# Kernel optimization log

Measured on AMD Instinct MI355X. Metric: run time of the kernel, lower is better.

## Reference

```python
import jax, jax.numpy as jnp
import numpy as np

D_MODEL = 1024
D_FF = 2 * D_MODEL
N_EXPERTS = 8
TOP_K = 2
SCAT_SCALE = 0.1


def setup_inputs() -> dict:
    key = jax.random.key(0)
    ks = jax.random.split(key, 8)
    s_in = 1.0 / np.sqrt(D_MODEL)
    s_ff = 1.0 / np.sqrt(D_FF)
    return {
        "x": jax.random.normal(ks[0], (4, 2048, D_MODEL), dtype=jnp.float32),
        "Wg": jax.random.uniform(ks[1], (D_MODEL, N_EXPERTS), minval=-s_in, maxval=s_in),
        "bg": jax.random.uniform(ks[2], (N_EXPERTS,), minval=-s_in, maxval=s_in),
        "W1": jax.random.uniform(ks[3], (N_EXPERTS, D_MODEL, D_FF), minval=-s_in, maxval=s_in),
        "b1": jax.random.uniform(ks[4], (N_EXPERTS, D_FF), minval=-s_in, maxval=s_in),
        "W2": jax.random.uniform(ks[5], (N_EXPERTS, D_FF, D_MODEL), minval=-s_ff, maxval=s_ff),
        "b2": jax.random.uniform(ks[6], (N_EXPERTS, D_MODEL), minval=-s_ff, maxval=s_ff),
    }


def reference(x, Wg, bg, W1, b1, W2, b2):
    B, N, D = x.shape
    T = B * N
    xf = x.reshape(T, D)

    # gating logits + norm-based modulation (scattering_scale branch)
    logits = xf @ Wg + bg  # [T, E]
    tnorm = jnp.linalg.norm(xf, axis=-1, keepdims=True)  # [T, 1]
    norm_scaled = (tnorm - tnorm.mean()) / (jnp.std(tnorm, ddof=1) + 1e-6)
    logits = logits + SCAT_SCALE * norm_scaled

    # top-k routing
    topv, topi = jax.lax.top_k(logits, TOP_K)  # [T, K]
    gates_k = jax.nn.softmax(topv, axis=-1)  # [T, K]
    routing_entropy = -(gates_k * jnp.log(jnp.clip(gates_k, 1e-8, None))).sum(-1).mean()

    # dense per-token expert-weight matrix (zeros for non-selected experts)
    E = W1.shape[0]
    gates = jnp.zeros((T, E), dtype=gates_k.dtype).at[
        jnp.arange(T)[:, None], topi
    ].add(gates_k)  # [T, E]

    # all-expert MLP (dense equivalent of sparse dispatch; weight 0 -> no contribution)
    h = jax.nn.relu(jnp.einsum("td,edf->etf", xf, W1) + b1[:, None, :])  # [E, T, F]
    y = jnp.einsum("etf,efd->etd", h, W2) + b2[:, None, :]  # [E, T, D]
    out = jnp.einsum("etd,te->td", y, gates).reshape(B, N, D)
    return out, routing_entropy
```

## Files before the change

kernel.cpp:

```cpp
#include <hip/hip_runtime.h>
#include <hip/hip_bf16.h>

#define T_TOK 8192
#define DMODEL 1024
#define DFF 2048
#define NEXP 8

typedef __attribute__((ext_vector_type(8))) short short8v;
typedef __attribute__((ext_vector_type(4))) float floatx4;
typedef __attribute__((ext_vector_type(4))) ushort ushort4v;

__device__ __forceinline__ ushort f2bf(float f) {
  union { float f; unsigned u; } v; v.f = f;
  unsigned u = v.u;
  unsigned r = (u + 0x7FFFu + ((u >> 16) & 1u)) >> 16;
  return (ushort)r;
}
__device__ __forceinline__ float bf2f(ushort b) {
  union { unsigned u; float f; } v; v.u = ((unsigned)b) << 16;
  return v.f;
}
__device__ __forceinline__ void gload16(const void* g, void* l) {
  __builtin_amdgcn_global_load_lds(
      (const __attribute__((address_space(1))) unsigned int*)g,
      (__attribute__((address_space(3))) unsigned int*)l, 16, 0, 0);
}
__device__ __forceinline__ short8v dsr128(unsigned off) {
  short8v r;
  asm volatile("ds_read_b128 %0, %1" : "=v"(r) : "v"(off));
  return r;
}
#define VMW(n) asm volatile("s_waitcnt vmcnt(" #n ")" ::: "memory")
#define LG0()  asm volatile("s_waitcnt lgkmcnt(0)" ::: "memory")
#define BAR()  asm volatile("s_barrier" ::: "memory")
#define SB0()  __builtin_amdgcn_sched_barrier(0)

__global__ void init_kernel(int* __restrict__ meta, float* __restrict__ entWs) {
  if (threadIdx.x < 64) meta[threadIdx.x] = 0;
  if (threadIdx.x == 0) *entWs = 0.f;
}

__global__ __launch_bounds__(256) void gating_kernel(
    const float* __restrict__ x, const float* __restrict__ Wg,
    const float* __restrict__ bg, int* __restrict__ meta,
    int* __restrict__ te, float* __restrict__ tg, float* __restrict__ entWs,
    ushort* __restrict__ xb) {
  __shared__ float wgT[8448];
  __shared__ float sbg[NEXP];
  __shared__ int cnt_s[NEXP];
  __shared__ float ent_s;
  int tid = threadIdx.x;
#pragma unroll
  for (int k = 0; k < 8; ++k) {
    int g4 = tid + 256 * k;
    float4 v = ((const float4*)Wg)[g4];
    int q = g4 * 4;
    int f = q >> 5;
    wgT[q + f]     = v.x;
    wgT[q + 1 + f] = v.y;
    wgT[q + 2 + f] = v.z;
    wgT[q + 3 + f] = v.w;
  }
  if (tid < NEXP) { sbg[tid] = bg[tid]; cnt_s[tid] = 0; }
  if (tid == 0) ent_s = 0.f;
  __syncthreads();

  int wid = tid >> 6, lane = tid & 63;
#pragma unroll 1
  for (int it = 0; it < 4; ++it) {
    int t = blockIdx.x * 16 + wid * 4 + it;
    const float* xr = x + (long)t * DMODEL;
    ushort* xbr = xb + (long)t * DMODEL;
    float acc[NEXP];
#pragma unroll
    for (int e = 0; e < NEXP; ++e) acc[e] = 0.f;
#pragma unroll
    for (int i = 0; i < 4; ++i) {
      int dbase = i * 256 + lane * 4;
      int pad = i * 64 + lane;
      float4 xv = *(const float4*)(xr + dbase);
      ushort4v s;
      s[0] = f2bf(xv.x); s[1] = f2bf(xv.y); s[2] = f2bf(xv.z); s[3] = f2bf(xv.w);
      *(ushort4v*)(xbr + dbase) = s;
      float xj[4] = {xv.x, xv.y, xv.z, xv.w};
#pragma unroll
      for (int j = 0; j < 4; ++j) {
        int base = 8 * (dbase + j) + pad;
#pragma unroll
        for (int e = 0; e < NEXP; ++e) acc[e] += xj[j] * wgT[base + e];
      }
    }
#pragma unroll
    for (int off = 32; off; off >>= 1)
#pragma unroll
      for (int e = 0; e < NEXP; ++e) acc[e] += __shfl_xor(acc[e], off, 64);
    if (lane == 0) {
      float lg[NEXP];
#pragma unroll
      for (int e = 0; e < NEXP; ++e) lg[e] = acc[e] + sbg[e];
      int e1 = 0; float v1 = lg[0];
#pragma unroll
      for (int e = 1; e < NEXP; ++e) if (lg[e] > v1) { v1 = lg[e]; e1 = e; }
      int e2 = -1; float v2 = -1e30f;
#pragma unroll
      for (int e = 0; e < NEXP; ++e) if (e != e1 && lg[e] > v2) { v2 = lg[e]; e2 = e; }
      float p2 = expf(v2 - v1);
      float s = 1.f + p2;
      float g1 = 1.f / s, g2 = p2 / s;
      float ent = -(g1 * logf(fmaxf(g1, 1e-8f)) + g2 * logf(fmaxf(g2, 1e-8f)));
      atomicAdd(&cnt_s[e1], 1);
      atomicAdd(&cnt_s[e2], 1);
      atomicAdd(&ent_s, ent);
      te[2 * t] = e1; te[2 * t + 1] = e2;
      tg[2 * t] = g1; tg[2 * t + 1] = g2;
    }
  }
  __syncthreads();
  if (tid < NEXP && cnt_s[tid]) atomicAdd(&meta[tid], cnt_s[tid]);
  if (tid == 0) atomicAdd(entWs, ent_s * (1.f / T_TOK));
}

__global__ void prefix_kernel(int* __restrict__ meta) {
  if (threadIdx.x == 0) {
    int s = 0;
    for (int e = 0; e < NEXP; ++e) { meta[16 + e] = s; s += meta[e]; meta[32 + e] = 0; }
  }
}

__global__ void scatter_kernel(const int* __restrict__ te, const float* __restrict__ tg,
                               int* __restrict__ meta, int* __restrict__ tok,
                               float* __restrict__ gate, int* __restrict__ slotOf) {
  int t = blockIdx.x * blockDim.x + threadIdx.x;
  if (t >= T_TOK) return;
  for (int k = 0; k < 2; ++k) {
    int e = te[2 * t + k];
    int pos = atomicAdd(&meta[32 + e], 1);
    int slot = meta[16 + e] + pos;
    tok[slot] = t;
    gate[slot] = tg[2 * t + k];
    slotOf[2 * t + k] = slot;
  }
}

__global__ __launch_bounds__(256) void tcvt_kernel(const float* __restrict__ src,
                                                   ushort* __restrict__ dst,
                                                   int R, int C) {
  __shared__ ushort tile[64][72];
  int tid = threadIdx.x;
  long eoff = (long)blockIdx.z * R * C;
  int r0 = blockIdx.y * 64, c0 = blockIdx.x * 64;
  int lr = tid >> 4, lc = (tid & 15) * 4;
#pragma unroll
  for (int p = 0; p < 4; ++p) {
    int r = lr + p * 16;
    float4 v = *(const float4*)&src[eoff + (long)(r0 + r) * C + (c0 + lc)];
    tile[r][lc + 0] = f2bf(v.x); tile[r][lc + 1] = f2bf(v.y);
    tile[r][lc + 2] = f2bf(v.z); tile[r][lc + 3] = f2bf(v.w);
  }
  __syncthreads();
  int sr = tid >> 3, sc = (tid & 7) * 8;
#pragma unroll
  for (int p = 0; p < 2; ++p) {
    int c = sr + p * 32;
    short8v v;
#pragma unroll
    for (int j = 0; j < 8; ++j) v[j] = (short)tile[sc + j][c];
    *(short8v*)&dst[eoff + (long)(c0 + c) * R + (r0 + sc)] = v;
  }
}

__device__ __forceinline__ void gemm_pipe(
    int NT, const char* aP0, const char* aP1,
    const char* bP0, const char* bP1, const char* bP2, const char* bP3,
    char* lds, int tid, floatx4 (&acc)[8][4]) {
  const unsigned ldsU = (unsigned)(unsigned long)lds;
  int lane = tid & 63, wid = tid >> 6;
  int lr = lane & 15, lg = lane >> 4;
  unsigned offA[8], offB[4];
#pragma unroll
  for (int mi = 0; mi < 8; ++mi) {
    int row = mi * 16 + lr;
    offA[mi] = row * 64 + ((lg * 16) ^ (((row >> 1) & 3) << 4));
  }
#pragma unroll
  for (int ni = 0; ni < 4; ++ni) {
    int row = wid * 64 + ni * 16 + lr;
    offB[ni] = row * 64 + ((lg * 16) ^ (((row >> 1) & 3) << 4));
  }

  auto STG = [&](int b, int t) {
    int koff = t * 64;
    char* da = lds + b * 8192;
    gload16(aP0 + koff, da + tid * 16);
    gload16(aP1 + koff, da + 4096 + tid * 16);
    char* db = lds + 24576 + b * 16384;
    gload16(bP0 + koff, db + tid * 16);
    gload16(bP1 + koff, db + 4096 + tid * 16);
    gload16(bP2 + koff, db + 8192 + tid * 16);
    gload16(bP3 + koff, db + 12288 + tid * 16);
  };
  auto RD = [&](int b, short8v (&af)[8], short8v (&bf)[4]) {
#pragma unroll
    for (int ni = 0; ni < 4; ++ni) bf[ni] = dsr128(ldsU + 24576u + (unsigned)(b * 16384) + offB[ni]);
#pragma unroll
    for (int mi = 0; mi < 8; ++mi) af[mi] = dsr128(ldsU + (unsigned)(b * 8192) + offA[mi]);
  };
  auto MM = [&](short8v (&af)[8], short8v (&bf)[4]) {
#pragma unroll
    for (int mi = 0; mi < 8; ++mi)
#pragma unroll
      for (int ni = 0; ni < 4; ++ni)
        acc[mi][ni] =
            __builtin_amdgcn_mfma_f32_16x16x32_bf16(af[mi], bf[ni], acc[mi][ni], 0, 0, 0);
  };

  STG(0, 0); STG(1, 1);
  VMW(6); BAR();

  short8v af[8], bf[4];
  int b = 0;
  for (int t = 0; t + 2 < NT; ++t) {
    RD(b, af, bf);
    int bs = (b == 0) ? 2 : b - 1;
    STG(bs, t + 2);
    VMW(6);
    BAR(); LG0(); SB0();
    __builtin_amdgcn_s_setprio(1); MM(af, bf); __builtin_amdgcn_s_setprio(0);
    SB0(); BAR();
    b = (b == 2) ? 0 : b + 1;
  }
  {
    RD(b, af, bf);
    VMW(0);
    BAR(); LG0(); SB0();
    __builtin_amdgcn_s_setprio(1); MM(af, bf); __builtin_amdgcn_s_setprio(0);
    SB0(); BAR();
    b = (b == 2) ? 0 : b + 1;
  }
  {
    RD(b, af, bf);
    LG0(); SB0();
    __builtin_amdgcn_s_setprio(1); MM(af, bf); __builtin_amdgcn_s_setprio(0);
  }
}

__global__ __launch_bounds__(256, 2) void gemm1_kernel(
    const ushort* __restrict__ xb, const ushort* __restrict__ w1t,
    const float* __restrict__ b1, const int* __restrict__ meta,
    const int* __restrict__ tok, ushort* __restrict__ h) {
  const int NWG = 64 * 8 * NEXP;
  int flat = blockIdx.x;
  int wgid = (flat % 8) * (NWG / 8) + flat / 8;
  int m0 = (wgid & 63) * 128;
  int rest = wgid >> 6;
  int n0 = (rest & 7) * 256;
  int e = rest >> 3;
  int cnt = meta[e];
  if (m0 >= cnt) return;
  int bas = meta[16 + e];
  __shared__ char lds[73728];
  int tid = threadIdx.x;

  const char* w1e = (const char*)(w1t + (long)e * DFF * DMODEL);
  int rA = tid >> 2;
  int ch = tid & 3;
  auto sc = [&](int row) { return (unsigned)((ch * 16) ^ (((row >> 1) & 3) << 4)); };
  int ma0 = m0 + rA;        if (ma0 >= cnt) ma0 = cnt - 1;
  int ma1 = m0 + rA + 64;   if (ma1 >= cnt) ma1 = cnt - 1;
  const char* aP0 = (const char*)xb + (long)tok[bas + ma0] * (DMODEL * 2) + sc(rA);
  const char* aP1 = (const char*)xb + (long)tok[bas + ma1] * (DMODEL * 2) + sc(rA + 64);
  const char* bP0 = w1e + (long)(n0 + rA) * (DMODEL * 2) + sc(rA);
  const char* bP1 = w1e + (long)(n0 + rA + 64) * (DMODEL * 2) + sc(rA + 64);
  const char* bP2 = w1e + (long)(n0 + rA + 128) * (DMODEL * 2) + sc(rA + 128);
  const char* bP3 = w1e + (long)(n0 + rA + 192) * (DMODEL * 2) + sc(rA + 192);

  floatx4 acc[8][4];
#pragma unroll
  for (int i = 0; i < 8; ++i)
#pragma unroll
    for (int j = 0; j < 4; ++j) acc[i][j] = (floatx4){0.f, 0.f, 0.f, 0.f};

  gemm_pipe(DMODEL / 32, aP0, aP1, bP0, bP1, bP2, bP3, lds, tid, acc);

  int lane = tid & 63, wid = tid >> 6;
  int lr = lane & 15, lg = lane >> 4;
  const float* b1e = b1 + e * DFF;
#pragma unroll
  for (int mi = 0; mi < 8; ++mi) {
#pragma unroll
    for (int r = 0; r < 4; ++r) {
      int m = m0 + mi * 16 + lg * 4 + r;
      if (m >= cnt) continue;
      long hrow = (long)(bas + m) * DFF;
#pragma unroll
      for (int ni = 0; ni < 4; ++ni) {
        int f = n0 + wid * 64 + ni * 16 + lr;
        float v = acc[mi][ni][r] + b1e[f];
        h[hrow + f] = f2bf(fmaxf(v, 0.f));
      }
    }
  }
}

__global__ __launch_bounds__(256, 2) void gemm2_kernel(
    const ushort* __restrict__ h, const ushort* __restrict__ w2t,
    const float* __restrict__ b2, const int* __restrict__ meta,
    const float* __restrict__ gate, ushort* __restrict__ y) {
  const int NWG = 64 * 4 * NEXP;
  int flat = blockIdx.x;
  int wgid = (flat % 8) * (NWG / 8) + flat / 8;
  int m0 = (wgid & 63) * 128;
  int rest = wgid >> 6;
  int n0 = (rest & 3) * 256;
  int e = rest >> 2;
  int cnt = meta[e];
  if (m0 >= cnt) return;
  int bas = meta[16 + e];
  __shared__ char lds[73728];
  int tid = threadIdx.x;

  const char* w2e = (const char*)(w2t + (long)e * DMODEL * DFF);
  int rA = tid >> 2;
  int ch = tid & 3;
  auto sc = [&](int row) { return (unsigned)((ch * 16) ^ (((row >> 1) & 3) << 4)); };
  int ma0 = m0 + rA;        if (ma0 >= cnt) ma0 = cnt - 1;
  int ma1 = m0 + rA + 64;   if (ma1 >= cnt) ma1 = cnt - 1;
  const char* aP0 = (const char*)h + (long)(bas + ma0) * (DFF * 2) + sc(rA);
  const char* aP1 = (const char*)h + (long)(bas + ma1) * (DFF * 2) + sc(rA + 64);
  const char* bP0 = w2e + (long)(n0 + rA) * (DFF * 2) + sc(rA);
  const char* bP1 = w2e + (long)(n0 + rA + 64) * (DFF * 2) + sc(rA + 64);
  const char* bP2 = w2e + (long)(n0 + rA + 128) * (DFF * 2) + sc(rA + 128);
  const char* bP3 = w2e + (long)(n0 + rA + 192) * (DFF * 2) + sc(rA + 192);

  floatx4 acc[8][4];
#pragma unroll
  for (int i = 0; i < 8; ++i)
#pragma unroll
    for (int j = 0; j < 4; ++j) acc[i][j] = (floatx4){0.f, 0.f, 0.f, 0.f};

  gemm_pipe(DFF / 32, aP0, aP1, bP0, bP1, bP2, bP3, lds, tid, acc);

  int lane = tid & 63, wid = tid >> 6;
  int lr = lane & 15, lg = lane >> 4;
  const float* b2e = b2 + e * DMODEL;
#pragma unroll
  for (int mi = 0; mi < 8; ++mi) {
#pragma unroll
    for (int r = 0; r < 4; ++r) {
      int m = m0 + mi * 16 + lg * 4 + r;
      if (m >= cnt) continue;
      int slot = bas + m;
      float g = gate[slot];
      ushort* yr = y + (long)slot * DMODEL;
#pragma unroll
      for (int ni = 0; ni < 4; ++ni) {
        int n = n0 + wid * 64 + ni * 16 + lr;
        float v = g * (acc[mi][ni][r] + b2e[n]);
        yr[n] = f2bf(v);
      }
    }
  }
}

__global__ __launch_bounds__(256) void combine_kernel(
    const ushort* __restrict__ y, const int* __restrict__ slotOf,
    const float* __restrict__ entWs, float* __restrict__ out) {
  int t = blockIdx.x;
  int s1 = slotOf[2 * t], s2 = slotOf[2 * t + 1];
  int d = threadIdx.x * 4;
  ushort4v a = *(const ushort4v*)&y[(long)s1 * DMODEL + d];
  ushort4v b = *(const ushort4v*)&y[(long)s2 * DMODEL + d];
  float4 r;
  r.x = bf2f(a[0]) + bf2f(b[0]);
  r.y = bf2f(a[1]) + bf2f(b[1]);
  r.z = bf2f(a[2]) + bf2f(b[2]);
  r.w = bf2f(a[3]) + bf2f(b[3]);
  *(float4*)&out[(long)t * DMODEL + d] = r;
  if (t == 0 && threadIdx.x == 0) out[(long)T_TOK * DMODEL] = *entWs;
}

extern "C" void kernel_launch(void* const* d_in, const int* in_sizes, int n_in,
                              void* d_out, int out_size, void* d_ws, size_t ws_size,
                              hipStream_t stream) {
  const float* x  = (const float*)d_in[0];
  const float* Wg = (const float*)d_in[1];
  const float* bg = (const float*)d_in[2];
  const float* W1 = (const float*)d_in[3];
  const float* b1 = (const float*)d_in[4];
  const float* W2 = (const float*)d_in[5];
  const float* b2 = (const float*)d_in[6];
  float* out = (float*)d_out;

  char* ws = (char*)d_ws;
  int*    meta   = (int*)(ws + 0);
  float*  entWs  = (float*)(ws + 256);
  int*    te     = (int*)(ws + 1024);
  float*  tg     = (float*)(ws + 66560);
  int*    tokA   = (int*)(ws + 132096);
  float*  gate   = (float*)(ws + 197632);
  int*    slotOf = (int*)(ws + 263168);
  ushort* xb     = (ushort*)(ws + 328704);
  ushort* w1t    = (ushort*)(ws + 17105920);
  ushort* w2t    = (ushort*)(ws + 50660352);
  ushort* h      = (ushort*)(ws + 84214784);
  ushort* y      = w1t;

  init_kernel<<<1, 64, 0, stream>>>(meta, entWs);
  gating_kernel<<<T_TOK / 16, 256, 0, stream>>>(x, Wg, bg, meta, te, tg, entWs, xb);
  prefix_kernel<<<1, 1, 0, stream>>>(meta);
  scatter_kernel<<<T_TOK / 256, 256, 0, stream>>>(te, tg, meta, tokA, gate, slotOf);
  tcvt_kernel<<<dim3(DFF / 64, DMODEL / 64, NEXP), 256, 0, stream>>>(W1, w1t, DMODEL, DFF);
  tcvt_kernel<<<dim3(DMODEL / 64, DFF / 64, NEXP), 256, 0, stream>>>(W2, w2t, DFF, DMODEL);
  gemm1_kernel<<<64 * 8 * NEXP, 256, 0, stream>>>(xb, w1t, b1, meta, tokA, h);
  gemm2_kernel<<<64 * 4 * NEXP, 256, 0, stream>>>(h, w2t, b2, meta, gate, y);
  combine_kernel<<<T_TOK, 256, 0, stream>>>(y, slotOf, entWs, out);
}
```

Baseline: 343.8 us.

## Shrink expert GEMM tiles to 128x128 with 2x2 wave layout and one-barrier pipeline

Both expert GEMMs drop from 128x256 to 128x128 output tiles, with the four waves arranged 2x2. This halves the accumulator registers and cuts LDS to 48KB, so the launch bound rises to 3 workgroups per CU and twice as many workgroups are launched. The triple-buffered main loop is restructured to use one barrier per iteration, and the two weight transpose/convert launches are merged into one. In exchange, each tile gets less operand reuse and global/LDS traffic per FLOP goes up.

```diff
diff --git a/kernel.cpp b/kernel.cpp
--- a/kernel.cpp
+++ b/kernel.cpp
@@ -142,13 +142,22 @@
   }
 }
 
-__global__ __launch_bounds__(256) void tcvt_kernel(const float* __restrict__ src,
-                                                   ushort* __restrict__ dst,
-                                                   int R, int C) {
+__global__ __launch_bounds__(256) void tcvt2_kernel(
+    const float* __restrict__ W1, const float* __restrict__ W2,
+    ushort* __restrict__ w1t, ushort* __restrict__ w2t) {
+  int id = blockIdx.x;
+  const float* src; ushort* dst; int R, C, r0, c0, e;
+  if (id < 4096) {
+    src = W1; dst = w1t; R = DMODEL; C = DFF;
+    c0 = (id & 31) * 64; r0 = ((id >> 5) & 15) * 64; e = id >> 9;
+  } else {
+    int j = id - 4096;
+    src = W2; dst = w2t; R = DFF; C = DMODEL;
+    c0 = (j & 15) * 64; r0 = ((j >> 4) & 31) * 64; e = j >> 9;
+  }
   __shared__ ushort tile[64][72];
   int tid = threadIdx.x;
-  long eoff = (long)blockIdx.z * R * C;
-  int r0 = blockIdx.y * 64, c0 = blockIdx.x * 64;
+  long eoff = (long)e * R * C;
   int lr = tid >> 4, lc = (tid & 15) * 4;
 #pragma unroll
   for (int p = 0; p < 4; ++p) {
@@ -170,21 +179,21 @@
 }
 
 __device__ __forceinline__ void gemm_pipe(
-    int NT, const char* aP0, const char* aP1,
-    const char* bP0, const char* bP1, const char* bP2, const char* bP3,
-    char* lds, int tid, floatx4 (&acc)[8][4]) {
+    int NT, const char* aP0, const char* aP1, const char* bP0, const char* bP1,
+    char* lds, int tid, floatx4 (&acc)[4][4]) {
   const unsigned ldsU = (unsigned)(unsigned long)lds;
   int lane = tid & 63, wid = tid >> 6;
   int lr = lane & 15, lg = lane >> 4;
-  unsigned offA[8], offB[4];
-#pragma unroll
-  for (int mi = 0; mi < 8; ++mi) {
-    int row = mi * 16 + lr;
+  int wm = (wid >> 1) * 64, wn = (wid & 1) * 64;
+  unsigned offA[4], offB[4];
+#pragma unroll
+  for (int mi = 0; mi < 4; ++mi) {
+    int row = wm + mi * 16 + lr;
     offA[mi] = row * 64 + ((lg * 16) ^ (((row >> 1) & 3) << 4));
   }
 #pragma unroll
   for (int ni = 0; ni < 4; ++ni) {
-    int row = wid * 64 + ni * 16 + lr;
+    int row = wn + ni * 16 + lr;
     offB[ni] = row * 64 + ((lg * 16) ^ (((row >> 1) & 3) << 4));
   }
 
@@ -193,21 +202,19 @@
     char* da = lds + b * 8192;
     gload16(aP0 + koff, da + tid * 16);
     gload16(aP1 + koff, da + 4096 + tid * 16);
-    char* db = lds + 24576 + b * 16384;
+    char* db = lds + 24576 + b * 8192;
     gload16(bP0 + koff, db + tid * 16);
     gload16(bP1 + koff, db + 4096 + tid * 16);
-    gload16(bP2 + koff, db + 8192 + tid * 16);
-    gload16(bP3 + koff, db + 12288 + tid * 16);
   };
-  auto RD = [&](int b, short8v (&af)[8], short8v (&bf)[4]) {
-#pragma unroll
-    for (int ni = 0; ni < 4; ++ni) bf[ni] = dsr128(ldsU + 24576u + (unsigned)(b * 16384) + offB[ni]);
-#pragma unroll
-    for (int mi = 0; mi < 8; ++mi) af[mi] = dsr128(ldsU + (unsigned)(b * 8192) + offA[mi]);
+  auto RD = [&](int b, short8v (&af)[4], short8v (&bf)[4]) {
+#pragma unroll
+    for (int ni = 0; ni < 4; ++ni) bf[ni] = dsr128(ldsU + 24576u + (unsigned)(b * 8192) + offB[ni]);
+#pragma unroll
+    for (int mi = 0; mi < 4; ++mi) af[mi] = dsr128(ldsU + (unsigned)(b * 8192) + offA[mi]);
   };
-  auto MM = [&](short8v (&af)[8], short8v (&bf)[4]) {
-#pragma unroll
-    for (int mi = 0; mi < 8; ++mi)
+  auto MM = [&](short8v (&af)[4], short8v (&bf)[4]) {
+#pragma unroll
+    for (int mi = 0; mi < 4; ++mi)
 #pragma unroll
       for (int ni = 0; ni < 4; ++ni)
         acc[mi][ni] =
@@ -215,50 +222,37 @@
   };
 
   STG(0, 0); STG(1, 1);
-  VMW(6); BAR();
-
-  short8v af[8], bf[4];
+
+  short8v af[4], bf[4];
   int b = 0;
-  for (int t = 0; t + 2 < NT; ++t) {
+#pragma unroll 1
+  for (int t = 0; t < NT; ++t) {
+    if (t == NT - 1) { VMW(0); } else { VMW(4); }
+    BAR();
     RD(b, af, bf);
-    int bs = (b == 0) ? 2 : b - 1;
-    STG(bs, t + 2);
-    VMW(6);
-    BAR(); LG0(); SB0();
-    __builtin_amdgcn_s_setprio(1); MM(af, bf); __builtin_amdgcn_s_setprio(0);
-    SB0(); BAR();
-    b = (b == 2) ? 0 : b + 1;
-  }
-  {
-    RD(b, af, bf);
-    VMW(0);
-    BAR(); LG0(); SB0();
-    __builtin_amdgcn_s_setprio(1); MM(af, bf); __builtin_amdgcn_s_setprio(0);
-    SB0(); BAR();
-    b = (b == 2) ? 0 : b + 1;
-  }
-  {
-    RD(b, af, bf);
+    if (t + 2 < NT) STG((b + 2 >= 3) ? b - 1 : b + 2, t + 2);
     LG0(); SB0();
     __builtin_amdgcn_s_setprio(1); MM(af, bf); __builtin_amdgcn_s_setprio(0);
-  }
-}
-
-__global__ __launch_bounds__(256, 2) void gemm1_kernel(
+    SB0();
+    b = (b == 2) ? 0 : b + 1;
+  }
+}
+
+__global__ __launch_bounds__(256, 3) void gemm1_kernel(
     const ushort* __restrict__ xb, const ushort* __restrict__ w1t,
     const float* __restrict__ b1, const int* __restrict__ meta,
     const int* __restrict__ tok, ushort* __restrict__ h) {
-  const int NWG = 64 * 8 * NEXP;
+  const int NWG = 64 * 16 * NEXP;
   int flat = blockIdx.x;
   int wgid = (flat % 8) * (NWG / 8) + flat / 8;
   int m0 = (wgid & 63) * 128;
   int rest = wgid >> 6;
-  int n0 = (rest & 7) * 256;
-  int e = rest >> 3;
+  int n0 = (rest & 15) * 128;
+  int e = rest >> 4;
   int cnt = meta[e];
   if (m0 >= cnt) return;
   int bas = meta[16 + e];
-  __shared__ char lds[73728];
+  __shared__ char lds[49152];
   int tid = threadIdx.x;
 
   const char* w1e = (const char*)(w1t + (long)e * DFF * DMODEL);
@@ -271,30 +265,29 @@
   const char* aP1 = (const char*)xb + (long)tok[bas + ma1] * (DMODEL * 2) + sc(rA + 64);
   const char* bP0 = w1e + (long)(n0 + rA) * (DMODEL * 2) + sc(rA);
   const char* bP1 = w1e + (long)(n0 + rA + 64) * (DMODEL * 2) + sc(rA + 64);
-  const char* bP2 = w1e + (long)(n0 + rA + 128) * (DMODEL * 2) + sc(rA + 128);
-  const char* bP3 = w1e + (long)(n0 + rA + 192) * (DMODEL * 2) + sc(rA + 192);
-
-  floatx4 acc[8][4];
-#pragma unroll
-  for (int i = 0; i < 8; ++i)
+
+  floatx4 acc[4][4];
+#pragma unroll
+  for (int i = 0; i < 4; ++i)
 #pragma unroll
     for (int j = 0; j < 4; ++j) acc[i][j] = (floatx4){0.f, 0.f, 0.f, 0.f};
 
-  gemm_pipe(DMODEL / 32, aP0, aP1, bP0, bP1, bP2, bP3, lds, tid, acc);
+  gemm_pipe(DMODEL / 32, aP0, aP1, bP0, bP1, lds, tid, acc);
 
   int lane = tid & 63, wid = tid >> 6;
   int lr = lane & 15, lg = lane >> 4;
+  int wm = (wid >> 1) * 64, wn = (wid & 1) * 64;
   const float* b1e = b1 + e * DFF;
 #pragma unroll
-  for (int mi = 0; mi < 8; ++mi) {
+  for (int mi = 0; mi < 4; ++mi) {
 #pragma unroll
     for (int r = 0; r < 4; ++r) {
-      int m = m0 + mi * 16 + lg * 4 + r;
+      int m = m0 + wm + mi * 16 + lg * 4 + r;
       if (m >= cnt) continue;
       long hrow = (long)(bas + m) * DFF;
 #pragma unroll
       for (int ni = 0; ni < 4; ++ni) {
-        int f = n0 + wid * 64 + ni * 16 + lr;
+        int f = n0 + wn + ni * 16 + lr;
         float v = acc[mi][ni][r] + b1e[f];
         h[hrow + f] = f2bf(fmaxf(v, 0.f));
       }
@@ -302,21 +295,21 @@
   }
 }
 
-__global__ __launch_bounds__(256, 2) void gemm2_kernel(
+__global__ __launch_bounds__(256, 3) void gemm2_kernel(
     const ushort* __restrict__ h, const ushort* __restrict__ w2t,
     const float* __restrict__ b2, const int* __restrict__ meta,
     const float* __restrict__ gate, ushort* __restrict__ y) {
-  const int NWG = 64 * 4 * NEXP;
+  const int NWG = 64 * 8 * NEXP;
   int flat = blockIdx.x;
   int wgid = (flat % 8) * (NWG / 8) + flat / 8;
   int m0 = (wgid & 63) * 128;
   int rest = wgid >> 6;
-  int n0 = (rest & 3) * 256;
-  int e = rest >> 2;
+  int n0 = (rest & 7) * 128;
+  int e = rest >> 3;
   int cnt = meta[e];
   if (m0 >= cnt) return;
   int bas = meta[16 + e];
-  __shared__ char lds[73728];
+  __shared__ char lds[49152];
   int tid = threadIdx.x;
 
   const char* w2e = (const char*)(w2t + (long)e * DMODEL * DFF);
@@ -329,32 +322,31 @@
   const char* aP1 = (const char*)h + (long)(bas + ma1) * (DFF * 2) + sc(rA + 64);
   const char* bP0 = w2e + (long)(n0 + rA) * (DFF * 2) + sc(rA);
   const char* bP1 = w2e + (long)(n0 + rA + 64) * (DFF * 2) + sc(rA + 64);
-  const char* bP2 = w2e + (long)(n0 + rA + 128) * (DFF * 2) + sc(rA + 128);
-  const char* bP3 = w2e + (long)(n0 + rA + 192) * (DFF * 2) + sc(rA + 192);
-
-  floatx4 acc[8][4];
-#pragma unroll
-  for (int i = 0; i < 8; ++i)
+
+  floatx4 acc[4][4];
+#pragma unroll
+  for (int i = 0; i < 4; ++i)
 #pragma unroll
     for (int j = 0; j < 4; ++j) acc[i][j] = (floatx4){0.f, 0.f, 0.f, 0.f};
 
-  gemm_pipe(DFF / 32, aP0, aP1, bP0, bP1, bP2, bP3, lds, tid, acc);
+  gemm_pipe(DFF / 32, aP0, aP1, bP0, bP1, lds, tid, acc);
 
   int lane = tid & 63, wid = tid >> 6;
   int lr = lane & 15, lg = lane >> 4;
+  int wm = (wid >> 1) * 64, wn = (wid & 1) * 64;
   const float* b2e = b2 + e * DMODEL;
 #pragma unroll
-  for (int mi = 0; mi < 8; ++mi) {
+  for (int mi = 0; mi < 4; ++mi) {
 #pragma unroll
     for (int r = 0; r < 4; ++r) {
-      int m = m0 + mi * 16 + lg * 4 + r;
+      int m = m0 + wm + mi * 16 + lg * 4 + r;
       if (m >= cnt) continue;
       int slot = bas + m;
       float g = gate[slot];
       ushort* yr = y + (long)slot * DMODEL;
 #pragma unroll
       for (int ni = 0; ni < 4; ++ni) {
-        int n = n0 + wid * 64 + ni * 16 + lr;
+        int n = n0 + wn + ni * 16 + lr;
         float v = g * (acc[mi][ni][r] + b2e[n]);
         yr[n] = f2bf(v);
       }
@@ -409,9 +401,8 @@
   gating_kernel<<<T_TOK / 16, 256, 0, stream>>>(x, Wg, bg, meta, te, tg, entWs, xb);
   prefix_kernel<<<1, 1, 0, stream>>>(meta);
   scatter_kernel<<<T_TOK / 256, 256, 0, stream>>>(te, tg, meta, tokA, gate, slotOf);
-  tcvt_kernel<<<dim3(DFF / 64, DMODEL / 64, NEXP), 256, 0, stream>>>(W1, w1t, DMODEL, DFF);
-  tcvt_kernel<<<dim3(DMODEL / 64, DFF / 64, NEXP), 256, 0, stream>>>(W2, w2t, DFF, DMODEL);
-  gemm1_kernel<<<64 * 8 * NEXP, 256, 0, stream>>>(xb, w1t, b1, meta, tokA, h);
-  gemm2_kernel<<<64 * 4 * NEXP, 256, 0, stream>>>(h, w2t, b2, meta, gate, y);
+  tcvt2_kernel<<<8192, 256, 0, stream>>>(W1, W2, w1t, w2t);
+  gemm1_kernel<<<64 * 16 * NEXP, 256, 0, stream>>>(xb, w1t, b1, meta, tokA, h);
+  gemm2_kernel<<<64 * 8 * NEXP, 256, 0, stream>>>(h, w2t, b2, meta, gate, y);
   combine_kernel<<<T_TOK, 256, 0, stream>>>(y, slotOf, entWs, out);
 }
```

After: 339.5 us. Within noise of the previous version (-1.3%).
